# Performance work log

Measured on AMD Instinct MI355X. Metric: run time of the kernel, lower is better.

The kernel has to match this reference:

```python
import jax, jax.numpy as jnp
import numpy as np

C_IN = 64
GDIM = C_IN // 2      # 32, GHPA dim_in
CD = GDIM // 4        # 8, c_dim_in
GRID = C_IN // 2      # 32, learned param grid (x=y)
EXPR = 2
B, W, H, D = 2, 64, 64, 64


def _gelu(x):
    return jax.nn.gelu(x, approximate=False)


def _interp_last(p, out_len):
    # 1D linear interpolation along last axis, align_corners=True
    L = p.shape[-1]
    pos = jnp.linspace(0.0, L - 1.0, out_len)
    i0 = jnp.clip(jnp.floor(pos).astype(jnp.int32), 0, L - 1)
    i1 = jnp.clip(i0 + 1, 0, L - 1)
    w = (pos - i0).astype(p.dtype)
    return p[..., i0] * (1.0 - w) + p[..., i1] * w


def _interp2(p, h, w):
    # bilinear align_corners=True over last two axes (separable)
    p = _interp_last(p, w)
    p = jnp.swapaxes(_interp_last(jnp.swapaxes(p, -2, -1), h), -2, -1)
    return p


def _conv2d(x, w, b, groups=1, pad=0):
    y = jax.lax.conv_general_dilated(x, w, (1, 1), [(pad, pad), (pad, pad)],
                                     feature_group_count=groups,
                                     dimension_numbers=('NCHW', 'OIHW', 'NCHW'))
    return y + b[None, :, None, None]


def _conv1d(x, w, b, groups=1, pad=0):
    y = jax.lax.conv_general_dilated(x, w, (1,), [(pad, pad)],
                                     feature_group_count=groups,
                                     dimension_numbers=('NCH', 'OIH', 'NCH'))
    return y + b[None, :, None]


def _ln_cf(x, g, b, eps=1e-6):
    # channels_first LayerNorm over channel axis 1 of NCHW
    u = x.mean(1, keepdims=True)
    s = ((x - u) ** 2).mean(1, keepdims=True)
    xh = (x - u) / jnp.sqrt(s + eps)
    return g[None, :, None, None] * xh + b[None, :, None, None]


def _inorm3d(x, eps=1e-5):
    # InstanceNorm3d, affine=False: normalize over spatial dims per (B, C)
    u = x.mean((2, 3, 4), keepdims=True)
    v = ((x - u) ** 2).mean((2, 3, 4), keepdims=True)
    return (x - u) / jnp.sqrt(v + eps)


def setup_inputs() -> dict:
    key = jax.random.key(0)
    ks = iter(jax.random.split(key, 40))
    f = lambda shape: 0.05 * jax.random.normal(next(ks), shape, dtype=jnp.float32)
    z = lambda shape: jnp.zeros(shape, jnp.float32)
    o = lambda shape: jnp.ones(shape, jnp.float32)
    inp = {
        'x': jax.random.normal(next(ks), (B, C_IN, W, H, D), dtype=jnp.float32),
        # GHPA layer norms
        'n1_g': o((GDIM,)), 'n1_b': z((GDIM,)),
        'n2_g': o((GDIM,)), 'n2_b': z((GDIM,)),
        # learned Hadamard params (torch inits to ones)
        'p_xy': o((1, CD, GRID, GRID)),
        'p_zx': o((1, 1, CD, GRID)),
        'p_zy': o((1, 1, CD, GRID)),
        # conv_xy: depthwise 3x3 + 1x1
        'xy_dw_w': f((CD, 1, 3, 3)), 'xy_dw_b': z((CD,)),
        'xy_pw_w': f((CD, CD, 1, 1)), 'xy_pw_b': z((CD,)),
        # conv_zx / conv_zy: depthwise 1d k=3 + 1x1 1d
        'zx_dw_w': f((CD, 1, 3)), 'zx_dw_b': z((CD,)),
        'zx_pw_w': f((CD, CD, 1)), 'zx_pw_b': z((CD,)),
        'zy_dw_w': f((CD, 1, 3)), 'zy_dw_b': z((CD,)),
        'zy_pw_w': f((CD, CD, 1)), 'zy_pw_b': z((CD,)),
        # dw branch: 1x1 + depthwise 3x3
        'dw_pw_w': f((CD, CD, 1, 1)), 'dw_pw_b': z((CD,)),
        'dw_dw_w': f((CD, 1, 3, 3)), 'dw_dw_b': z((CD,)),
        # ldw: depthwise 3x3 + 1x1 on full GDIM
        'ldw_dw_w': f((GDIM, 1, 3, 3)), 'ldw_dw_b': z((GDIM,)),
        'ldw_pw_w': f((GDIM, GDIM, 1, 1)), 'ldw_pw_b': z((GDIM,)),
        # MlpChannel 1x1x1 convs as dense over channel
        'fc1_w': f((C_IN * EXPR, C_IN)), 'fc1_b': z((C_IN * EXPR,)),
        'fc2_w': f((C_IN, C_IN * EXPR)), 'fc2_b': z((C_IN,)),
    }
    return inp


def reference(x, n1_g, n1_b, n2_g, n2_b, p_xy, p_zx, p_zy,
              xy_dw_w, xy_dw_b, xy_pw_w, xy_pw_b,
              zx_dw_w, zx_dw_b, zx_pw_w, zx_pw_b,
              zy_dw_w, zy_dw_b, zy_pw_w, zy_pw_b,
              dw_pw_w, dw_pw_b, dw_dw_w, dw_dw_b,
              ldw_dw_w, ldw_dw_b, ldw_pw_w, ldw_pw_b,
              fc1_w, fc1_b, fc2_w, fc2_b):
    cd = CD

    def ghpa(z):  # z: (N, GDIM, A, Bd)
        N, C, A, Bd = z.shape
        z = _ln_cf(z, n1_g, n1_b)
        x1, x2, x3, x4 = jnp.split(z, 4, axis=1)
        # xy branch: interpolate learned 2D grid, conv, Hadamard
        k = _interp2(p_xy, A, Bd)                       # (1, cd, A, Bd)
        k = _conv2d(k, xy_dw_w, xy_dw_b, groups=cd, pad=1)
        k = _conv2d(_gelu(k), xy_pw_w, xy_pw_b)
        x1 = x1 * k
        # zx branch: permute (N,cd,A,Bd)->(N,Bd,cd,A)
        x2p = jnp.transpose(x2, (0, 3, 1, 2))
        kz = _interp2(p_zx, cd, A)[0]                   # (1, cd, A)
        kz = _conv1d(kz, zx_dw_w, zx_dw_b, groups=cd, pad=1)
        kz = _conv1d(_gelu(kz), zx_pw_w, zx_pw_b)
        x2 = jnp.transpose(x2p * kz[None], (0, 2, 3, 1))
        # zy branch: permute (N,cd,A,Bd)->(N,A,cd,Bd)
        x3p = jnp.transpose(x3, (0, 2, 1, 3))
        ky = _interp2(p_zy, cd, Bd)[0]                  # (1, cd, Bd)
        ky = _conv1d(ky, zy_dw_w, zy_dw_b, groups=cd, pad=1)
        ky = _conv1d(_gelu(ky), zy_pw_w, zy_pw_b)
        x3 = jnp.transpose(x3p * ky[None], (0, 2, 1, 3))
        # dw branch
        x4 = _conv2d(x4, dw_pw_w, dw_pw_b)
        x4 = _conv2d(_gelu(x4), dw_dw_w, dw_dw_b, groups=cd, pad=1)
        z = jnp.concatenate([x1, x2, x3, x4], axis=1)
        z = _ln_cf(z, n2_g, n2_b)
        z = _conv2d(z, ldw_dw_w, ldw_dw_b, groups=GDIM, pad=1)
        z = _conv2d(_gelu(z), ldw_pw_w, ldw_pw_b)
        return z

    xh, xres = jnp.split(x, 2, axis=1)                  # each (B, GDIM, W, H, D)
    xh = _inorm3d(xh)
    Bb, C, Ww, Hh, Dd = xh.shape
    # direction 0: 'b c w h d -> (h b) c w d'
    xr = jnp.transpose(xh, (3, 0, 1, 2, 4)).reshape(Hh * Bb, C, Ww, Dd)
    y1 = ghpa(xr).reshape(Hh, Bb, C, Ww, Dd).transpose(1, 2, 3, 0, 4)
    y2 = ghpa(xr[::-1]).reshape(Hh, Bb, C, Ww, Dd).transpose(1, 2, 3, 0, 4)[::-1]
    whd = y1 + y2
    z = jnp.concatenate([whd, xres], axis=1)            # (B, C_IN, W, H, D)
    z = _inorm3d(z)
    # MlpChannel: 1x1x1 convs = channel-wise dense
    h = jnp.einsum('bcwhd,oc->bowhd', z, fc1_w) + fc1_b[None, :, None, None, None]
    h = _gelu(h)
    out = jnp.einsum('bcwhd,oc->bowhd', h, fc2_w) + fc2_b[None, :, None, None, None]
    return out
```

## Files before the change

### kernel.cpp

```cpp
#include <hip/hip_runtime.h>
#include <hip/hip_bf16.h>

typedef __hip_bfloat16 bf16;
typedef __attribute__((ext_vector_type(8))) short short8;
typedef __attribute__((ext_vector_type(4))) float f32x4;

__device__ __forceinline__ float b2f(bf16 v){ return __bfloat162float(v); }
__device__ __forceinline__ bf16  f2b(float v){ return __float2bfloat16(v); }
__device__ __forceinline__ unsigned short f2bu(float f){
  return __builtin_bit_cast(unsigned short, __float2bfloat16(f));
}
__device__ __forceinline__ float u2f(unsigned short u){
  return __uint_as_float(((unsigned int)u) << 16);
}
__device__ __forceinline__ float geluf(float x){ return 0.5f*x*(1.0f+erff(x*0.70710678118654752440f)); }

template<bool F32> __device__ __forceinline__ float ldin(const void* p, size_t i){
  if (F32) return ((const float*)p)[i];
  return b2f(((const bf16*)p)[i]);
}
__device__ __forceinline__ float ldf(const void* p, size_t i, bool f32){
  return f32 ? ((const float*)p)[i] : b2f(((const bf16*)p)[i]);
}

#define SS    4096
#define SSS   262144

__global__ void k_probe(const unsigned short* __restrict__ xr, int* __restrict__ flag){
  float m = 0.f;
  for (int i = threadIdx.x; i < 512; i += 64){
    unsigned int u = ((unsigned int)xr[i]) << 16;
    float v = fabsf(__uint_as_float(u));
    if (!(v < 3.0e38f)) v = 3.0e38f;
    m = fmaxf(m, v);
  }
  #pragma unroll
  for (int off = 32; off > 0; off >>= 1) m = fmaxf(m, __shfl_down(m, off));
  if (threadIdx.x == 0) flag[0] = (m > 1000.0f) ? 1 : 0;
}

__device__ __forceinline__ void blk_reduce2(float& s, float& s2){
  __shared__ float sa[4], sb[4];
  #pragma unroll
  for (int off = 32; off > 0; off >>= 1){ s += __shfl_down(s, off); s2 += __shfl_down(s2, off); }
  int wid = threadIdx.x >> 6;
  if ((threadIdx.x & 63) == 0){ sa[wid] = s; sb[wid] = s2; }
  __syncthreads();
  if (threadIdx.x == 0){ s = sa[0]+sa[1]+sa[2]+sa[3]; s2 = sb[0]+sb[1]+sb[2]+sb[3]; }
}

__global__ __launch_bounds__(256) void k_cstats(const int* __restrict__ flag,
    const void* __restrict__ x, float* __restrict__ part){
  const bool f32 = (flag[0] != 0);
  int bc = blockIdx.x >> 3, sp = blockIdx.x & 7;
  size_t base = (size_t)bc*SSS + (size_t)sp*32768;
  float s = 0.f, s2 = 0.f;
  if (f32){
    const float4* p = (const float4*)((const float*)x + base);
    for (int i = threadIdx.x; i < 8192; i += 256){
      float4 v = p[i];
      s += v.x+v.y+v.z+v.w; s2 += v.x*v.x+v.y*v.y+v.z*v.z+v.w*v.w;
    }
  } else {
    const ushort4* p = (const ushort4*)((const unsigned short*)x + base);
    for (int i = threadIdx.x; i < 8192; i += 256){
      ushort4 v = p[i];
      float a=u2f(v.x),b_=u2f(v.y),c=u2f(v.z),d=u2f(v.w);
      s += a+b_+c+d; s2 += a*a+b_*b_+c*c+d*d;
    }
  }
  blk_reduce2(s, s2);
  if (threadIdx.x == 0){ part[blockIdx.x*2] = s; part[blockIdx.x*2+1] = s2; }
}

__global__ void k_sfinal(const float* __restrict__ part,
    float* __restrict__ meanH, float* __restrict__ rstdH,
    float* __restrict__ mean2, float* __restrict__ rstd2){
  int t = threadIdx.x; if (t >= 128) return;
  float s = 0.f, s2 = 0.f;
  #pragma unroll
  for (int i = 0; i < 8; i++){ s += part[(t*8+i)*2]; s2 += part[(t*8+i)*2+1]; }
  float m = s * (1.f/262144.f);
  float var = s2 * (1.f/262144.f) - m*m;
  int b = t >> 6, c = t & 63;
  if (c < 32){ meanH[b*32+c] = m; rstdH[b*32+c] = rsqrtf(var + 1e-5f); }
  else       { mean2[t] = m;      rstd2[t] = rsqrtf(var + 1e-5f); }
}

__global__ __launch_bounds__(256) void k_mult1(const int* __restrict__ flag,
    const void* __restrict__ p_xy, const void* __restrict__ p_zx, const void* __restrict__ p_zy,
    const void* __restrict__ xy_dw_w, const void* __restrict__ xy_dw_b,
    const void* __restrict__ zx_dw_w, const void* __restrict__ zx_dw_b,
    const void* __restrict__ zy_dw_w, const void* __restrict__ zy_dw_b,
    float* __restrict__ t_xy, float* __restrict__ t_zx, float* __restrict__ t_zy){
  const bool f32 = (flag[0] != 0);
  const float SC = 31.f/63.f;
  int id = blockIdx.x*256 + threadIdx.x;
  if (id < 32768){
    int c = id >> 12, rem = id & 4095, uu = rem >> 6, vv = rem & 63;
    float acc = ldf(xy_dw_b, c, f32);
    for (int du = 0; du < 3; du++){
      int ui = uu + du - 1; if (ui < 0 || ui >= 64) continue;
      float pu = ui*SC; int i0 = (int)pu; float wu = pu - (float)i0; int i1 = min(i0+1, 31);
      for (int dv = 0; dv < 3; dv++){
        int vi = vv + dv - 1; if (vi < 0 || vi >= 64) continue;
        float pv = vi*SC; int j0 = (int)pv; float wv = pv - (float)j0; int j1 = min(j0+1, 31);
        float s = ldf(p_xy, c*1024+i0*32+j0, f32)*(1.f-wu)*(1.f-wv) + ldf(p_xy, c*1024+i0*32+j1, f32)*(1.f-wu)*wv
                + ldf(p_xy, c*1024+i1*32+j0, f32)*wu*(1.f-wv)       + ldf(p_xy, c*1024+i1*32+j1, f32)*wu*wv;
        acc += ldf(xy_dw_w, c*9 + du*3 + dv, f32) * s;
      }
    }
    t_xy[id] = geluf(acc);
  } else if (id < 33280){
    int k = id - 32768; int c = k >> 6, a = k & 63;
    float acc = ldf(zx_dw_b, c, f32);
    for (int da = 0; da < 3; da++){
      int ai = a + da - 1; if (ai < 0 || ai >= 64) continue;
      float pa = ai*SC; int i0 = (int)pa; float wa = pa - (float)i0; int i1 = min(i0+1, 31);
      float s = ldf(p_zx, c*32+i0, f32)*(1.f-wa) + ldf(p_zx, c*32+i1, f32)*wa;
      acc += ldf(zx_dw_w, c*3+da, f32) * s;
    }
    t_zx[k] = geluf(acc);
  } else if (id < 33792){
    int k = id - 33280; int c = k >> 6, a = k & 63;
    float acc = ldf(zy_dw_b, c, f32);
    for (int da = 0; da < 3; da++){
      int ai = a + da - 1; if (ai < 0 || ai >= 64) continue;
      float pa = ai*SC; int i0 = (int)pa; float wa = pa - (float)i0; int i1 = min(i0+1, 31);
      float s = ldf(p_zy, c*32+i0, f32)*(1.f-wa) + ldf(p_zy, c*32+i1, f32)*wa;
      acc += ldf(zy_dw_w, c*3+da, f32) * s;
    }
    t_zy[k] = geluf(acc);
  }
}

__global__ __launch_bounds__(256) void k_mult2(const int* __restrict__ flag,
    const float* __restrict__ t_xy, const float* __restrict__ t_zx, const float* __restrict__ t_zy,
    const void* __restrict__ xy_pw_w, const void* __restrict__ xy_pw_b,
    const void* __restrict__ zx_pw_w, const void* __restrict__ zx_pw_b,
    const void* __restrict__ zy_pw_w, const void* __restrict__ zy_pw_b,
    float* __restrict__ kxy, float* __restrict__ kz, float* __restrict__ ky){
  const bool f32 = (flag[0] != 0);
  int id = blockIdx.x*256 + threadIdx.x;
  if (id < 32768){
    int oc = id >> 12, pix = id & 4095;
    float acc = ldf(xy_pw_b, oc, f32);
    #pragma unroll
    for (int ic = 0; ic < 8; ic++) acc += ldf(xy_pw_w, oc*8+ic, f32) * t_xy[ic*4096 + pix];
    kxy[id] = acc;
  } else if (id < 33280){
    int k = id - 32768; int oc = k >> 6, a = k & 63;
    float acc = ldf(zx_pw_b, oc, f32);
    #pragma unroll
    for (int ic = 0; ic < 8; ic++) acc += ldf(zx_pw_w, oc*8+ic, f32) * t_zx[ic*64 + a];
    kz[k] = acc;
  } else if (id < 33792){
    int k = id - 33280; int oc = k >> 6, a = k & 63;
    float acc = ldf(zy_pw_b, oc, f32);
    #pragma unroll
    for (int ic = 0; ic < 8; ic++) acc += ldf(zy_pw_w, oc*8+ic, f32) * t_zy[ic*64 + a];
    ky[k] = acc;
  }
}

#define TB 4
#define W_M    0
#define W_R    32
#define W_G1   64
#define W_B1   96
#define W_G2   128
#define W_B2   160
#define W_LDWB 192
#define W_LPWB 224
#define W_PW   256
#define W_PWB  320
#define W_DW   328
#define W_DWB  400
#define W_LDW  408
#define W_LPW  696
#define W_TOT  1720

template<bool F32>
__global__ __launch_bounds__(256, 3) void k_g(const int* __restrict__ flag,
    const void* __restrict__ x,
    const void* n1g_, const void* n1b_, const void* n2g_, const void* n2b_,
    const void* dwpw_w, const void* dwpw_b, const void* dwdw_w, const void* dwdw_b,
    const void* ldw_dw_w, const void* ldw_dw_b, const void* ldw_pw_w, const void* ldw_pw_b,
    const float* __restrict__ meanH, const float* __restrict__ rstdH,
    const float* __restrict__ kxy, const float* __restrict__ kz, const float* __restrict__ ky,
    bf16* __restrict__ g){
  if (flag[0] != (F32 ? 1 : 0)) return;
  __shared__ unsigned short t4g[8*8*64];
  __shared__ unsigned short vln[32*6*64];
  __shared__ float sw[W_TOT];
  int n  = blockIdx.x >> 4;
  int a0 = (blockIdx.x & 15) * TB;
  int b = n & 1, h = n >> 1;
  int t = threadIdx.x;
  if (t < 32){
    sw[W_M+t]=meanH[b*32+t]; sw[W_R+t]=rstdH[b*32+t];
    sw[W_G1+t]=ldin<F32>(n1g_, t); sw[W_B1+t]=ldin<F32>(n1b_, t);
    sw[W_G2+t]=ldin<F32>(n2g_, t); sw[W_B2+t]=ldin<F32>(n2b_, t);
    sw[W_LDWB+t]=ldin<F32>(ldw_dw_b, t); sw[W_LPWB+t]=ldin<F32>(ldw_pw_b, t);
  }
  if (t >= 64 && t < 128) sw[W_PW+t-64]=ldin<F32>(dwpw_w, t-64);
  if (t >= 128 && t < 200) sw[W_DW+t-128]=ldin<F32>(dwdw_w, t-128);
  if (t >= 200 && t < 208) sw[W_PWB+t-200]=ldin<F32>(dwpw_b, t-200);
  if (t >= 208 && t < 216) sw[W_DWB+t-208]=ldin<F32>(dwdw_b, t-208);
  for (int i = t; i < 288; i += 256)  sw[W_LDW+i] = ldin<F32>(ldw_dw_w, i);
  for (int i = t; i < 1024; i += 256) sw[W_LPW+i] = ldin<F32>(ldw_pw_w, i);
  __syncthreads();
  const float* s_m = sw+W_M; const float* s_r = sw+W_R;
  const float* s_g1 = sw+W_G1; const float* s_b1 = sw+W_B1;
  const float* s_g2 = sw+W_G2; const float* s_b2 = sw+W_B2;
  const size_t xbase = (size_t)b*64*SSS + (size_t)h*64;

  for (int p = t; p < 8*64; p += 256){
    int row = p >> 6, d = p & 63;
    int a = a0 - 2 + row;
    if (a < 0 || a >= 64){
      #pragma unroll
      for (int ic = 0; ic < 8; ic++) t4g[(ic*8+row)*64+d] = 0;
      continue;
    }
    size_t xi = xbase + (size_t)a*SS + d;
    float sum = 0.f, sq = 0.f; float z24[8];
    #pragma unroll
    for (int c = 0; c < 32; c++){
      float v = (ldin<F32>(x, xi + (size_t)c*SSS) - s_m[c]) * s_r[c];
      sum += v; sq += v*v;
      if (c >= 24) z24[c-24] = v;
    }
    float mu = sum * (1.f/32.f);
    float inv = rsqrtf(sq*(1.f/32.f) - mu*mu + 1e-6f);
    float zl[8];
    #pragma unroll
    for (int j = 0; j < 8; j++) zl[j] = (z24[j]-mu)*inv*s_g1[24+j] + s_b1[24+j];
    #pragma unroll
    for (int ic = 0; ic < 8; ic++){
      float acc = sw[W_PWB+ic];
      #pragma unroll
      for (int j = 0; j < 8; j++) acc += sw[W_PW+ic*8+j]*zl[j];
      t4g[(ic*8+row)*64+d] = f2bu(geluf(acc));
    }
  }
  __syncthreads();

  for (int p = t; p < 6*64; p += 256){
    int row = p >> 6, d = p & 63;
    int a = a0 - 1 + row;
    if (a < 0 || a >= 64){
      #pragma unroll
      for (int c = 0; c < 32; c++) vln[(c*6+row)*64+d] = 0;
      continue;
    }
    size_t xi = xbase + (size_t)a*SS + d;
    float sum = 0.f, sq = 0.f;
    #pragma unroll
    for (int c = 0; c < 32; c++){
      float v = (ldin<F32>(x, xi + (size_t)c*SSS) - s_m[c]) * s_r[c];
      sum += v; sq += v*v;
    }
    float mu = sum * (1.f/32.f);
    float inv = rsqrtf(sq*(1.f/32.f) - mu*mu + 1e-6f);
    float s2 = 0.f, q2 = 0.f;
    #pragma unroll
    for (int c = 0; c < 8; c++){
      float v = (ldin<F32>(x, xi + (size_t)c*SSS) - s_m[c]) * s_r[c];
      float u = ((v-mu)*inv*s_g1[c] + s_b1[c]) * kxy[(c*64 + a)*64 + d];
      vln[(c*6+row)*64+d] = f2bu(u); s2 += u; q2 += u*u;
    }
    #pragma unroll
    for (int c = 8; c < 16; c++){
      float v = (ldin<F32>(x, xi + (size_t)c*SSS) - s_m[c]) * s_r[c];
      float u = ((v-mu)*inv*s_g1[c] + s_b1[c]) * kz[(c-8)*64 + a];
      vln[(c*6+row)*64+d] = f2bu(u); s2 += u; q2 += u*u;
    }
    #pragma unroll
    for (int c = 16; c < 24; c++){
      float v = (ldin<F32>(x, xi + (size_t)c*SSS) - s_m[c]) * s_r[c];
      float u = ((v-mu)*inv*s_g1[c] + s_b1[c]) * ky[(c-16)*64 + d];
      vln[(c*6+row)*64+d] = f2bu(u); s2 += u; q2 += u*u;
    }
    #pragma unroll
    for (int oc = 0; oc < 8; oc++){
      float acc = sw[W_DWB+oc];
      #pragma unroll
      for (int du = 0; du < 3; du++){
        #pragma unroll
        for (int dv = 0; dv < 3; dv++){
          int v2 = d + dv - 1;
          if (v2 >= 0 && v2 < 64) acc += sw[W_DW+oc*9+du*3+dv]*u2f(t4g[(oc*8+row+du)*64+v2]);
        }
      }
      vln[((24+oc)*6+row)*64+d] = f2bu(acc); s2 += acc; q2 += acc*acc;
    }
    float mu2 = s2 * (1.f/32.f);
    float inv2 = rsqrtf(q2*(1.f/32.f) - mu2*mu2 + 1e-6f);
    #pragma unroll
    for (int c = 0; c < 32; c++){
      int idx = (c*6+row)*64+d;
      float uu = u2f(vln[idx]);
      vln[idx] = f2bu((uu-mu2)*inv2*s_g2[c] + s_b2[c]);
    }
  }
  __syncthreads();

  for (int p = t; p < TB*64; p += 256){
    int row = p >> 6, d = p & 63;
    int a = a0 + row;
    float gd[32];
    #pragma unroll
    for (int oc = 0; oc < 32; oc++){
      float acc = sw[W_LDWB+oc];
      #pragma unroll
      for (int du = 0; du < 3; du++){
        #pragma unroll
        for (int dv = 0; dv < 3; dv++){
          int v2 = d + dv - 1;
          if (v2 >= 0 && v2 < 64) acc += sw[W_LDW+oc*9+du*3+dv]*u2f(vln[(oc*6+row+du)*64+v2]);
        }
      }
      gd[oc] = geluf(acc);
    }
    bf16* gp = g + (size_t)n*131072 + (size_t)a*64 + d;
    #pragma unroll
    for (int o = 0; o < 32; o++){
      float acc = sw[W_LPWB+o];
      #pragma unroll
      for (int ic = 0; ic < 32; ic++) acc += sw[W_LPW+o*32+ic]*gd[ic];
      gp[(size_t)o*4096] = f2b(acc);
    }
  }
}

__global__ __launch_bounds__(256) void k_gstats(const bf16* __restrict__ g,
                                                float* __restrict__ partg){
  int pair = blockIdx.x >> 3, sp = blockIdx.x & 7;
  int b = pair >> 5, c = pair & 31;
  float s = 0.f, s2 = 0.f;
  for (int i = threadIdx.x; i < 32768; i += 256){
    int ii = sp*32768 + i;
    int d = ii & 63, w = (ii >> 6) & 63, h = ii >> 12;
    int n1 = h*2 + b, n2 = (63-h)*2 + b;
    float v = b2f(g[((size_t)n1*32 + c)*4096 + w*64 + d]) + b2f(g[((size_t)n2*32 + c)*4096 + w*64 + d]);
    s += v; s2 += v*v;
  }
  blk_reduce2(s, s2);
  if (threadIdx.x == 0){ partg[blockIdx.x*2] = s; partg[blockIdx.x*2+1] = s2; }
}

__global__ void k_gfinal(const float* __restrict__ partg,
                         float* __restrict__ mean2, float* __restrict__ rstd2){
  int t = threadIdx.x; if (t >= 64) return;
  float s = 0.f, s2 = 0.f;
  #pragma unroll
  for (int i = 0; i < 8; i++){ s += partg[(t*8+i)*2]; s2 += partg[(t*8+i)*2+1]; }
  float m = s * (1.f/262144.f);
  float var = s2 * (1.f/262144.f) - m*m;
  int b = t >> 5, c = t & 31;
  mean2[b*64+c] = m; rstd2[b*64+c] = rsqrtf(var + 1e-5f);
}

__global__ __launch_bounds__(256) void k_mlp(const int* __restrict__ flag,
    const void* __restrict__ x, const bf16* __restrict__ g,
    const float* __restrict__ mean2, const float* __restrict__ rstd2,
    const void* __restrict__ fc1w, const void* __restrict__ fc1b,
    const void* __restrict__ fc2w, const void* __restrict__ fc2b,
    void* __restrict__ out){
  const bool f32 = (flag[0] != 0);
  __shared__ unsigned short zs[128*72];
  __shared__ unsigned short w1s[128*72];
  __shared__ unsigned short w2s[64*136];
  __shared__ unsigned short hb[4*16*136];
  __shared__ float b1s[128], b2s[64];
  int blk = blockIdx.x;
  int b = blk >> 11, w = (blk >> 5) & 63, hblk = blk & 31;
  int h0 = hblk*2;
  int t = threadIdx.x;
  const float* m2 = mean2 + b*64;
  const float* r2 = rstd2 + b*64;

  if (f32){
    const float* W1 = (const float*)fc1w;
    const float* W2 = (const float*)fc2w;
    for (int i = t; i < 8192; i += 256){ int j = i >> 6, c = i & 63; w1s[j*72+c] = f2bu(W1[i] * r2[c]); }
    for (int i = t; i < 8192; i += 256){ int o = i >> 7, j = i & 127; w2s[o*136+j] = f2bu(W2[i]); }
    if (t < 128){
      float s = 0.f;
      for (int c = 0; c < 64; c++) s += W1[t*64+c] * m2[c] * r2[c];
      b1s[t] = ((const float*)fc1b)[t] - s;
    }
    if (t < 64) b2s[t] = ((const float*)fc2b)[t];
  } else {
    const bf16* W1 = (const bf16*)fc1w;
    const bf16* W2 = (const bf16*)fc2w;
    for (int i = t; i < 8192; i += 256){ int j = i >> 6, c = i & 63; w1s[j*72+c] = f2bu(b2f(W1[i]) * r2[c]); }
    for (int i = t; i < 8192; i += 256){ int o = i >> 7, j = i & 127; w2s[o*136+j] = f2bu(b2f(W2[i])); }
    if (t < 128){
      float s = 0.f;
      for (int c = 0; c < 64; c++) s += b2f(W1[t*64+c]) * m2[c] * r2[c];
      b1s[t] = b2f(((const bf16*)fc1b)[t]) - s;
    }
    if (t < 64) b2s[t] = b2f(((const bf16*)fc2b)[t]);
  }

  {
    int px = t & 127, half = t >> 7;
    int hh = px >> 6, d = px & 63;
    int h = h0 + hh;
    unsigned short tmp[32];
    if (half == 0){
      int n1 = h*2 + b, n2 = (63-h)*2 + b;
      const bf16* g1 = g + ((size_t)n1*32)*4096 + w*64 + d;
      const bf16* g2 = g + ((size_t)n2*32)*4096 + w*64 + d;
      #pragma unroll
      for (int c = 0; c < 32; c++) tmp[c] = f2bu(b2f(g1[(size_t)c*4096]) + b2f(g2[(size_t)c*4096]));
    } else {
      size_t xi = ((size_t)(b*64+32))*SSS + (size_t)w*4096 + (size_t)h*64 + d;
      if (f32){
        const float* xp = (const float*)x;
        #pragma unroll
        for (int c = 0; c < 32; c++) tmp[c] = f2bu(xp[xi + (size_t)c*SSS]);
      } else {
        const unsigned short* xp = (const unsigned short*)x;
        #pragma unroll
        for (int c = 0; c < 32; c++) tmp[c] = xp[xi + (size_t)c*SSS];
      }
    }
    short8* dst = (short8*)&zs[px*72 + half*32];
    #pragma unroll
    for (int q = 0; q < 4; q++) dst[q] = *(short8*)&tmp[q*8];
  }
  __syncthreads();

  int wv = t >> 6, l = t & 63;
  int lr = l & 15, lg = l >> 4;
  unsigned short* hbw = &hb[wv*16*136];
  #pragma unroll
  for (int mi = 0; mi < 2; mi++){
    int px0 = wv*32 + mi*16;
    short8 a0 = *(const short8*)&zs[(px0+lr)*72 + lg*8];
    short8 a1 = *(const short8*)&zs[(px0+lr)*72 + 32 + lg*8];
    f32x4 acc[8];
    #pragma unroll
    for (int jt = 0; jt < 8; jt++){
      short8 b0 = *(const short8*)&w1s[(jt*16+lr)*72 + lg*8];
      short8 b1 = *(const short8*)&w1s[(jt*16+lr)*72 + 32 + lg*8];
      f32x4 c4 = {0.f,0.f,0.f,0.f};
      c4 = __builtin_amdgcn_mfma_f32_16x16x32_bf16(a0, b0, c4, 0, 0, 0);
      c4 = __builtin_amdgcn_mfma_f32_16x16x32_bf16(a1, b1, c4, 0, 0, 0);
      acc[jt] = c4;
    }
    #pragma unroll
    for (int jt = 0; jt < 8; jt++){
      float bj = b1s[jt*16+lr];
      #pragma unroll
      for (int r = 0; r < 4; r++){
        hbw[(lg*4+r)*136 + jt*16 + lr] = f2bu(geluf(acc[jt][r] + bj));
      }
    }
    short8 ha[4];
    #pragma unroll
    for (int m = 0; m < 4; m++) ha[m] = *(const short8*)&hbw[lr*136 + m*32 + lg*8];
    #pragma unroll
    for (int ot = 0; ot < 4; ot++){
      f32x4 c4 = {0.f,0.f,0.f,0.f};
      #pragma unroll
      for (int m = 0; m < 4; m++){
        short8 bb = *(const short8*)&w2s[(ot*16+lr)*136 + m*32 + lg*8];
        c4 = __builtin_amdgcn_mfma_f32_16x16x32_bf16(ha[m], bb, c4, 0, 0, 0);
      }
      int oc = ot*16 + lr;
      float bo = b2s[oc];
      if (f32){
        float* op = (float*)out;
        #pragma unroll
        for (int r = 0; r < 4; r++){
          int px = px0 + lg*4 + r;
          size_t oi = ((size_t)(b*64+oc))*SSS + (size_t)w*4096 + (size_t)(h0 + (px>>6))*64 + (px&63);
          op[oi] = c4[r] + bo;
        }
      } else {
        bf16* op = (bf16*)out;
        #pragma unroll
        for (int r = 0; r < 4; r++){
          int px = px0 + lg*4 + r;
          size_t oi = ((size_t)(b*64+oc))*SSS + (size_t)w*4096 + (size_t)(h0 + (px>>6))*64 + (px&63);
          op[oi] = f2b(c4[r] + bo);
        }
      }
    }
  }
}

extern "C" void kernel_launch(void* const* d_in, const int* in_sizes, int n_in,
                              void* d_out, int out_size, void* d_ws, size_t ws_size,
                              hipStream_t stream) {
  const void* X      = d_in[0];
  const void* n1g    = d_in[1];
  const void* n1b    = d_in[2];
  const void* n2g    = d_in[3];
  const void* n2b    = d_in[4];
  const void* p_xy   = d_in[5];
  const void* p_zx   = d_in[6];
  const void* p_zy   = d_in[7];
  const void* xy_dw_w= d_in[8];
  const void* xy_dw_b= d_in[9];
  const void* xy_pw_w= d_in[10];
  const void* xy_pw_b= d_in[11];
  const void* zx_dw_w= d_in[12];
  const void* zx_dw_b= d_in[13];
  const void* zx_pw_w= d_in[14];
  const void* zx_pw_b= d_in[15];
  const void* zy_dw_w= d_in[16];
  const void* zy_dw_b= d_in[17];
  const void* zy_pw_w= d_in[18];
  const void* zy_pw_b= d_in[19];
  const void* dw_pw_w= d_in[20];
  const void* dw_pw_b= d_in[21];
  const void* dw_dw_w= d_in[22];
  const void* dw_dw_b= d_in[23];
  const void* ldw_dw_w=d_in[24];
  const void* ldw_dw_b=d_in[25];
  const void* ldw_pw_w=d_in[26];
  const void* ldw_pw_b=d_in[27];
  const void* fc1w   = d_in[28];
  const void* fc1b   = d_in[29];
  const void* fc2w   = d_in[30];
  const void* fc2b   = d_in[31];

  int*  flag = (int*)d_ws;
  bf16* g    = (bf16*)((char*)d_ws + 16);
  float* fb  = (float*)((char*)d_ws + 16 + (size_t)16777216*2);
  float* meanH = fb;
  float* rstdH = fb + 64;
  float* t_xy  = fb + 128;
  float* t_zx  = fb + 32896;
  float* t_zy  = fb + 33408;
  float* kxy   = fb + 33920;
  float* kz    = fb + 66688;
  float* ky    = fb + 67200;
  float* mean2 = fb + 67712;
  float* rstd2 = fb + 67840;
  float* part  = fb + 67968;
  float* partg = fb + 70016;

  k_probe<<<1, 64, 0, stream>>>((const unsigned short*)X, flag);
  k_cstats<<<1024, 256, 0, stream>>>(flag, X, part);
  k_sfinal<<<1, 128, 0, stream>>>(part, meanH, rstdH, mean2, rstd2);
  k_mult1<<<132, 256, 0, stream>>>(flag, p_xy, p_zx, p_zy, xy_dw_w, xy_dw_b,
                                   zx_dw_w, zx_dw_b, zy_dw_w, zy_dw_b, t_xy, t_zx, t_zy);
  k_mult2<<<132, 256, 0, stream>>>(flag, t_xy, t_zx, t_zy, xy_pw_w, xy_pw_b,
                                   zx_pw_w, zx_pw_b, zy_pw_w, zy_pw_b, kxy, kz, ky);
  k_g<false><<<128*(64/TB), 256, 0, stream>>>(flag, X, n1g, n1b, n2g, n2b,
                                       dw_pw_w, dw_pw_b, dw_dw_w, dw_dw_b,
                                       ldw_dw_w, ldw_dw_b, ldw_pw_w, ldw_pw_b,
                                       meanH, rstdH, kxy, kz, ky, g);
  k_g<true ><<<128*(64/TB), 256, 0, stream>>>(flag, X, n1g, n1b, n2g, n2b,
                                       dw_pw_w, dw_pw_b, dw_dw_w, dw_dw_b,
                                       ldw_dw_w, ldw_dw_b, ldw_pw_w, ldw_pw_b,
                                       meanH, rstdH, kxy, kz, ky, g);
  k_gstats<<<512, 256, 0, stream>>>(g, partg);
  k_gfinal<<<1, 64, 0, stream>>>(partg, mean2, rstd2);
  k_mlp<<<4096, 256, 0, stream>>>(flag, X, g, mean2, rstd2, fc1w, fc1b, fc2w, fc2b, d_out);
}
```

Before: 458.9 us.

## Stage normalized input tile in shared memory and reuse it across phases

The k_g kernel now loads its 8-row input halo tile once with vectorized float4/ushort4 loads. It applies the instance-norm mean/rstd and keeps the result as bf16 in a shared buffer. Phases 1 and 2 read from this buffer instead of reloading x from global memory up to three times per element. Phase 2 writes its layer-norm output in place, replacing the separate vln array. The minimum-blocks launch bound is also dropped, which lets the compiler use more registers, at some risk to occupancy. The bf16 staging adds rounding before the first layer norm.

```diff
diff --git a/kernel.cpp b/kernel.cpp
--- a/kernel.cpp
+++ b/kernel.cpp
@@ -181,7 +181,7 @@
 #define W_TOT  1720
 
 template<bool F32>
-__global__ __launch_bounds__(256, 3) void k_g(const int* __restrict__ flag,
+__global__ __launch_bounds__(256) void k_g(const int* __restrict__ flag,
     const void* __restrict__ x,
     const void* n1g_, const void* n1b_, const void* n2g_, const void* n2b_,
     const void* dwpw_w, const void* dwpw_b, const void* dwdw_w, const void* dwdw_b,
@@ -190,8 +190,8 @@
     const float* __restrict__ kxy, const float* __restrict__ kz, const float* __restrict__ ky,
     bf16* __restrict__ g){
   if (flag[0] != (F32 ? 1 : 0)) return;
+  __shared__ unsigned short xs[32*8*64];
   __shared__ unsigned short t4g[8*8*64];
-  __shared__ unsigned short vln[32*6*64];
   __shared__ float sw[W_TOT];
   int n  = blockIdx.x >> 4;
   int a0 = (blockIdx.x & 15) * TB;
@@ -210,32 +210,52 @@
   for (int i = t; i < 288; i += 256)  sw[W_LDW+i] = ldin<F32>(ldw_dw_w, i);
   for (int i = t; i < 1024; i += 256) sw[W_LPW+i] = ldin<F32>(ldw_pw_w, i);
   __syncthreads();
-  const float* s_m = sw+W_M; const float* s_r = sw+W_R;
   const float* s_g1 = sw+W_G1; const float* s_b1 = sw+W_B1;
   const float* s_g2 = sw+W_G2; const float* s_b2 = sw+W_B2;
+  const int arow0 = a0 - 2;
   const size_t xbase = (size_t)b*64*SSS + (size_t)h*64;
+
+  for (int i = t; i < 4096; i += 256){
+    int c = i >> 7, row = (i >> 4) & 7, q = i & 15;
+    int a = arow0 + row;
+    unsigned short o0=0,o1=0,o2=0,o3=0;
+    if (a >= 0 && a < 64){
+      float m = sw[W_M+c], r = sw[W_R+c];
+      size_t base = xbase + (size_t)c*SSS + (size_t)a*SS + q*4;
+      if (F32){
+        float4 v = *(const float4*)((const float*)x + base);
+        o0=f2bu((v.x-m)*r); o1=f2bu((v.y-m)*r); o2=f2bu((v.z-m)*r); o3=f2bu((v.w-m)*r);
+      } else {
+        ushort4 v = *(const ushort4*)((const unsigned short*)x + base);
+        o0=f2bu((u2f(v.x)-m)*r); o1=f2bu((u2f(v.y)-m)*r); o2=f2bu((u2f(v.z)-m)*r); o3=f2bu((u2f(v.w)-m)*r);
+      }
+    }
+    ushort4 o4; o4.x=o0; o4.y=o1; o4.z=o2; o4.w=o3;
+    *(ushort4*)&xs[(c*8+row)*64 + q*4] = o4;
+  }
+  __syncthreads();
 
   for (int p = t; p < 8*64; p += 256){
     int row = p >> 6, d = p & 63;
-    int a = a0 - 2 + row;
+    int a = arow0 + row;
     if (a < 0 || a >= 64){
       #pragma unroll
       for (int ic = 0; ic < 8; ic++) t4g[(ic*8+row)*64+d] = 0;
       continue;
     }
-    size_t xi = xbase + (size_t)a*SS + d;
-    float sum = 0.f, sq = 0.f; float z24[8];
+    float sum = 0.f, sq = 0.f;
     #pragma unroll
     for (int c = 0; c < 32; c++){
-      float v = (ldin<F32>(x, xi + (size_t)c*SSS) - s_m[c]) * s_r[c];
-      sum += v; sq += v*v;
-      if (c >= 24) z24[c-24] = v;
+      float v = u2f(xs[(c*8+row)*64+d]); sum += v; sq += v*v;
     }
     float mu = sum * (1.f/32.f);
     float inv = rsqrtf(sq*(1.f/32.f) - mu*mu + 1e-6f);
     float zl[8];
     #pragma unroll
-    for (int j = 0; j < 8; j++) zl[j] = (z24[j]-mu)*inv*s_g1[24+j] + s_b1[24+j];
+    for (int j = 0; j < 8; j++){
+      float v = u2f(xs[((24+j)*8+row)*64+d]);
+      zl[j] = (v-mu)*inv*s_g1[24+j] + s_b1[24+j];
+    }
     #pragma unroll
     for (int ic = 0; ic < 8; ic++){
       float acc = sw[W_PWB+ic];
@@ -247,40 +267,35 @@
   __syncthreads();
 
   for (int p = t; p < 6*64; p += 256){
-    int row = p >> 6, d = p & 63;
-    int a = a0 - 1 + row;
-    if (a < 0 || a >= 64){
-      #pragma unroll
-      for (int c = 0; c < 32; c++) vln[(c*6+row)*64+d] = 0;
-      continue;
-    }
-    size_t xi = xbase + (size_t)a*SS + d;
+    int r2 = p >> 6, d = p & 63;
+    int a = a0 - 1 + r2;
+    if (a < 0 || a >= 64) continue;
+    int row = r2 + 1;
     float sum = 0.f, sq = 0.f;
     #pragma unroll
     for (int c = 0; c < 32; c++){
-      float v = (ldin<F32>(x, xi + (size_t)c*SSS) - s_m[c]) * s_r[c];
-      sum += v; sq += v*v;
+      float v = u2f(xs[(c*8+row)*64+d]); sum += v; sq += v*v;
     }
     float mu = sum * (1.f/32.f);
     float inv = rsqrtf(sq*(1.f/32.f) - mu*mu + 1e-6f);
     float s2 = 0.f, q2 = 0.f;
     #pragma unroll
     for (int c = 0; c < 8; c++){
-      float v = (ldin<F32>(x, xi + (size_t)c*SSS) - s_m[c]) * s_r[c];
-      float u = ((v-mu)*inv*s_g1[c] + s_b1[c]) * kxy[(c*64 + a)*64 + d];
-      vln[(c*6+row)*64+d] = f2bu(u); s2 += u; q2 += u*u;
+      int idx = (c*8+row)*64+d;
+      float u = ((u2f(xs[idx])-mu)*inv*s_g1[c] + s_b1[c]) * kxy[(c*64 + a)*64 + d];
+      xs[idx] = f2bu(u); s2 += u; q2 += u*u;
     }
     #pragma unroll
     for (int c = 8; c < 16; c++){
-      float v = (ldin<F32>(x, xi + (size_t)c*SSS) - s_m[c]) * s_r[c];
-      float u = ((v-mu)*inv*s_g1[c] + s_b1[c]) * kz[(c-8)*64 + a];
-      vln[(c*6+row)*64+d] = f2bu(u); s2 += u; q2 += u*u;
+      int idx = (c*8+row)*64+d;
+      float u = ((u2f(xs[idx])-mu)*inv*s_g1[c] + s_b1[c]) * kz[(c-8)*64 + a];
+      xs[idx] = f2bu(u); s2 += u; q2 += u*u;
     }
     #pragma unroll
     for (int c = 16; c < 24; c++){
-      float v = (ldin<F32>(x, xi + (size_t)c*SSS) - s_m[c]) * s_r[c];
-      float u = ((v-mu)*inv*s_g1[c] + s_b1[c]) * ky[(c-16)*64 + d];
-      vln[(c*6+row)*64+d] = f2bu(u); s2 += u; q2 += u*u;
+      int idx = (c*8+row)*64+d;
+      float u = ((u2f(xs[idx])-mu)*inv*s_g1[c] + s_b1[c]) * ky[(c-16)*64 + d];
+      xs[idx] = f2bu(u); s2 += u; q2 += u*u;
     }
     #pragma unroll
     for (int oc = 0; oc < 8; oc++){
@@ -290,25 +305,25 @@
         #pragma unroll
         for (int dv = 0; dv < 3; dv++){
           int v2 = d + dv - 1;
-          if (v2 >= 0 && v2 < 64) acc += sw[W_DW+oc*9+du*3+dv]*u2f(t4g[(oc*8+row+du)*64+v2]);
+          if (v2 >= 0 && v2 < 64) acc += sw[W_DW+oc*9+du*3+dv]*u2f(t4g[(oc*8+r2+du)*64+v2]);
         }
       }
-      vln[((24+oc)*6+row)*64+d] = f2bu(acc); s2 += acc; q2 += acc*acc;
+      xs[((24+oc)*8+row)*64+d] = f2bu(acc); s2 += acc; q2 += acc*acc;
     }
     float mu2 = s2 * (1.f/32.f);
     float inv2 = rsqrtf(q2*(1.f/32.f) - mu2*mu2 + 1e-6f);
     #pragma unroll
     for (int c = 0; c < 32; c++){
-      int idx = (c*6+row)*64+d;
-      float uu = u2f(vln[idx]);
-      vln[idx] = f2bu((uu-mu2)*inv2*s_g2[c] + s_b2[c]);
+      int idx = (c*8+row)*64+d;
+      float uu = u2f(xs[idx]);
+      xs[idx] = f2bu((uu-mu2)*inv2*s_g2[c] + s_b2[c]);
     }
   }
   __syncthreads();
 
-  for (int p = t; p < TB*64; p += 256){
-    int row = p >> 6, d = p & 63;
-    int a = a0 + row;
+  {
+    int r = t >> 6, d = t & 63;
+    int a = a0 + r;
     float gd[32];
     #pragma unroll
     for (int oc = 0; oc < 32; oc++){
@@ -318,7 +333,7 @@
         #pragma unroll
         for (int dv = 0; dv < 3; dv++){
           int v2 = d + dv - 1;
-          if (v2 >= 0 && v2 < 64) acc += sw[W_LDW+oc*9+du*3+dv]*u2f(vln[(oc*6+row+du)*64+v2]);
+          if (v2 >= 0 && v2 < 64) acc += sw[W_LDW+oc*9+du*3+dv]*u2f(xs[(oc*8+r+1+du)*64+v2]);
         }
       }
       gd[oc] = geluf(acc);
```

Measured after the change: 392.7 us. 1.17x faster.
